# Kernel optimization log

Hardware: AMD Instinct MI355X
Metric: run time of the kernel (lower is better)

## Reference

```python
import jax, jax.numpy as jnp
import numpy as np

BATCH = 2048
INPUT_DIM = 256    # == output_units, since Dense output is fed back into the cell
DEC_UNITS = 1024
OUTPUT_STEPS = 96
OUTPUT_UNITS = 256


def setup_inputs() -> dict:
    key = jax.random.key(0)
    ks = jax.random.split(key, 8)
    scale = 0.05
    return {
        "last_input": jax.random.normal(ks[0], (BATCH, INPUT_DIM), dtype=jnp.float32),
        "h0": jax.random.normal(ks[1], (BATCH, DEC_UNITS), dtype=jnp.float32),
        "c0": jax.random.normal(ks[2], (BATCH, DEC_UNITS), dtype=jnp.float32),
        # LSTMCell params (Keras layout: kernel [in, 4*units], recurrent_kernel [units, 4*units], bias [4*units]; gate order i,f,c,o)
        "Wk": jax.random.normal(ks[3], (INPUT_DIM, 4 * DEC_UNITS), dtype=jnp.float32) * scale,
        "Wr": jax.random.normal(ks[4], (DEC_UNITS, 4 * DEC_UNITS), dtype=jnp.float32) * scale,
        "b": jax.random.normal(ks[5], (4 * DEC_UNITS,), dtype=jnp.float32) * scale,
        # Dense output projection
        "Wd": jax.random.normal(ks[6], (DEC_UNITS, OUTPUT_UNITS), dtype=jnp.float32) * scale,
        "bd": jax.random.normal(ks[7], (OUTPUT_UNITS,), dtype=jnp.float32) * scale,
    }


def reference(last_input, h0, c0, Wk, Wr, b, Wd, bd):
    def step(carry, _):
        x, h, c = carry
        # fused gate GEMM: [B, in] @ [in, 4U] + [B, U] @ [U, 4U]
        z = x @ Wk + h @ Wr + b
        zi, zf, zg, zo = jnp.split(z, 4, axis=-1)  # Keras gate order: i, f, c(g), o
        i = jax.nn.sigmoid(zi)
        f = jax.nn.sigmoid(zf)
        o = jax.nn.sigmoid(zo)
        c_new = f * c + i * jnp.tanh(zg)
        h_new = o * jnp.tanh(c_new)
        pred = h_new @ Wd + bd  # fed back as next step's input
        return (pred, h_new, c_new), pred

    _, preds = jax.lax.scan(step, (last_input, h0, c0), None, length=OUTPUT_STEPS)
    # preds: [T, B, out] -> [B, T, out] (matches tf.transpose(predictions, [1,0,2]))
    return jnp.transpose(preds, (1, 0, 2))
```

## Files before the change

### kernel.cpp

```cpp
#include <hip/hip_runtime.h>
#include <hip/hip_bf16.h>
#include <stdint.h>

#define B_SZ 2048
#define U_SZ 1024
#define G_SZ 4096
#define I_SZ 256
#define O_SZ 256
#define T_SZ 96
#define K1_SZ 1280

typedef _Float16 half8 __attribute__((ext_vector_type(8)));
typedef float float4v __attribute__((ext_vector_type(4)));

__device__ inline float sigm_f(float x) { return 1.0f / (1.0f + __expf(-x)); }
__device__ inline float tanh_f(float x) { return 1.0f - 2.0f / (1.0f + __expf(2.0f * x)); }

__device__ inline short f2h(float x) {
    return __builtin_bit_cast(short, (_Float16)x);
}

__device__ inline void cp16(const void* g, void* l) {
    __builtin_amdgcn_global_load_lds(
        (const __attribute__((address_space(1))) void*)g,
        (__attribute__((address_space(3))) void*)l,
        16, 0, 0);
}


__global__ void transpose_reord(const float* __restrict__ in, float* __restrict__ out, int K) {
    __shared__ float s[32][33];
    int c0 = blockIdx.x * 32, k0 = blockIdx.y * 32;
    int tx = threadIdx.x, ty = threadIdx.y;
#pragma unroll
    for (int i = 0; i < 4; i++)
        s[ty + 8 * i][tx] = in[(long)(k0 + ty + 8 * i) * G_SZ + c0 + tx];
    __syncthreads();
#pragma unroll
    for (int i = 0; i < 4; i++) {
        int cc = ty + 8 * i;
        int c = c0 + cc;
        int n = 4 * (c & 1023) + (c >> 10);
        out[(long)n * K + k0 + tx] = s[tx][cc];
    }
}

__global__ void transpose_f32(const float* __restrict__ in, float* __restrict__ out, int R, int C) {
    __shared__ float s[32][33];
    int c0 = blockIdx.x * 32, r0 = blockIdx.y * 32;
    int tx = threadIdx.x, ty = threadIdx.y;
#pragma unroll
    for (int i = 0; i < 4; i++)
        s[ty + 8 * i][tx] = in[(long)(r0 + ty + 8 * i) * C + c0 + tx];
    __syncthreads();
#pragma unroll
    for (int i = 0; i < 4; i++)
        out[(long)(c0 + ty + 8 * i) * R + r0 + tx] = s[tx][ty + 8 * i];
}

__global__ void transpose_f16(const float* __restrict__ in, short* __restrict__ out, int R, int C) {
    __shared__ float s[32][33];
    int c0 = blockIdx.x * 32, r0 = blockIdx.y * 32;
    int tx = threadIdx.x, ty = threadIdx.y;
#pragma unroll
    for (int i = 0; i < 4; i++)
        s[ty + 8 * i][tx] = in[(long)(r0 + ty + 8 * i) * C + c0 + tx];
    __syncthreads();
#pragma unroll
    for (int i = 0; i < 4; i++)
        out[(long)(c0 + ty + 8 * i) * R + r0 + tx] = f2h(s[tx][ty + 8 * i]);
}

__global__ void cast_f16(const float* __restrict__ in, short* __restrict__ out) {
    long i = (long)blockIdx.x * 256 + threadIdx.x;
    out[i] = f2h(in[i]);
}

__global__ void build_b0t(const float* __restrict__ WkT, const float* __restrict__ WrT,
                          short* __restrict__ B0T) {
    long idx = (long)blockIdx.x * 256 + threadIdx.x;
    long n = idx / K1_SZ, k = idx % K1_SZ;
    float v = (k < I_SZ) ? WkT[n * I_SZ + k] : WrT[n * U_SZ + (k - I_SZ)];
    B0T[idx] = f2h(v);
}

__global__ void build_x0(const float* __restrict__ x0, const float* __restrict__ h0,
                         short* __restrict__ X0) {
    long idx = (long)blockIdx.x * 256 + threadIdx.x;
    long m = idx / K1_SZ, k = idx % K1_SZ;
    float v = (k < I_SZ) ? x0[m * I_SZ + k] : h0[m * U_SZ + (k - I_SZ)];
    X0[idx] = f2h(v);
}

__global__ void build_ber(const float* __restrict__ Wk, const float* __restrict__ b,
                          const float* __restrict__ bd, float* __restrict__ beR,
                          float* __restrict__ bR) {
    int c = blockIdx.x * 256 + threadIdx.x;
    float s = 0.0f;
    for (int p = 0; p < I_SZ; p++) s += bd[p] * Wk[(long)p * G_SZ + c];
    int slot = 4 * (c & 1023) + (c >> 10);
    bR[slot] = b[c];
    beR[slot] = b[c] + s;
}

__device__ __forceinline__ void gemm_core(char* smem, const char* gA, const char* gB,
                                          long Kb, int KI, int w, int l,
                                          float4v (&acc)[4][4]) {
    const int lr = l & 15, lk = l >> 4;
    const int wg = w >> 1, wb = w & 1;
    char* const lA = smem + (w * 32) * 128;
    char* const lB = smem + 32768 + (w * 16) * 128;

    auto stage = [&](int kt, int b) {
        const long go = (long)kt * 128;
        char* dA = lA + b * 49152;
        char* dB = lB + b * 49152;
#pragma unroll
        for (int ci = 0; ci < 4; ++ci) cp16(gA + (long)ci * 8 * Kb + go, dA + ci * 1024);
#pragma unroll
        for (int ci = 0; ci < 2; ++ci) cp16(gB + (long)ci * 8 * Kb + go, dB + ci * 1024);
    };
    auto compute = [&](int b) {
        const char* As = smem + b * 49152;
        const char* Bs = As + 32768;
#pragma unroll
        for (int ks = 0; ks < 2; ++ks) {
            half8 af[4], bf[4];
            const int chunk = (ks * 4 + lk) ^ (lr & 7);
#pragma unroll
            for (int mi = 0; mi < 4; ++mi)
                af[mi] = *(const half8*)(As + (wg * 64 + mi * 16 + lr) * 128 + chunk * 16);
#pragma unroll
            for (int ni = 0; ni < 4; ++ni)
                bf[ni] = *(const half8*)(Bs + (wb * 64 + ni * 16 + lr) * 128 + chunk * 16);
            __builtin_amdgcn_s_setprio(1);
#pragma unroll
            for (int mi = 0; mi < 4; ++mi)
#pragma unroll
                for (int ni = 0; ni < 4; ++ni)
                    acc[mi][ni] = __builtin_amdgcn_mfma_f32_16x16x32_f16(
                        af[mi], bf[ni], acc[mi][ni], 0, 0, 0);
            __builtin_amdgcn_s_setprio(0);
        }
    };

    stage(0, 0);
    stage(1, 1);
    int bc = 0, bs = 2;
    for (int kt = 0; kt < KI; ++kt) {
        if (kt < KI - 1)
            asm volatile("s_waitcnt vmcnt(6) lgkmcnt(0)" ::: "memory");
        else
            asm volatile("s_waitcnt vmcnt(0) lgkmcnt(0)" ::: "memory");
        __builtin_amdgcn_s_barrier();
        asm volatile("" ::: "memory");
        if (kt + 2 < KI) stage(kt + 2, bs);
        compute(bc);
        bc = (bc == 2) ? 0 : bc + 1;
        bs = (bs == 2) ? 0 : bs + 1;
    }
}

__global__ __launch_bounds__(512, 2) void lstm_step(
    const short* __restrict__ A, const short* __restrict__ Bm, int K,
    float* __restrict__ cT, const float* __restrict__ beR, short* __restrict__ hOut) {
    __shared__ char smem[147456];

    const int tid = threadIdx.x;
    const int w = tid >> 6, l = tid & 63;
    const int wg = w >> 1, wb = w & 1;
    const int n_blk = blockIdx.x, m_blk = blockIdx.y;
    const long Kb = (long)K * 2;

    float4v acc[4][4];
#pragma unroll
    for (int i = 0; i < 4; i++)
#pragma unroll
        for (int j = 0; j < 4; j++) acc[i][j] = (float4v)0.0f;

    const int r8 = l >> 3;
    const int s8 = l & 7;
    const int gch = s8 ^ r8;
    const char* gA = (const char*)A + ((long)(n_blk * 256 + w * 32 + r8)) * Kb + gch * 16;
    const char* gB = (const char*)Bm + ((long)(m_blk * 128 + w * 16 + r8)) * Kb + gch * 16;

    gemm_core(smem, gA, gB, Kb, K >> 6, w, l, acc);

    const int lr = l & 15, lk = l >> 4;
    short* hs = (short*)smem;
    __syncthreads();
    const int j_base = n_blk * 64 + wg * 16;
    const int m_base = m_blk * 128 + wb * 64;
#pragma unroll
    for (int mi = 0; mi < 4; ++mi) {
        int j = j_base + mi * 4 + lk;
        float4v bias = *(const float4v*)(beR + 4 * j);
#pragma unroll
        for (int ni = 0; ni < 4; ++ni) {
            int m = m_base + ni * 16 + lr;
            float zi = acc[mi][ni][0] + bias[0];
            float zf = acc[mi][ni][1] + bias[1];
            float zg = acc[mi][ni][2] + bias[2];
            float zo = acc[mi][ni][3] + bias[3];
            float ig = sigm_f(zi), fg = sigm_f(zf), gg = tanh_f(zg), og = sigm_f(zo);
            long cidx = (long)j * B_SZ + m;
            float cn = fg * cT[cidx] + ig * gg;
            cT[cidx] = cn;
            float h = og * tanh_f(cn);
            int mm = wb * 64 + ni * 16 + lr;
            int jj = wg * 16 + mi * 4 + lk;
            hs[mm * 64 + (jj ^ ((mm & 7) << 3))] = f2h(h);
        }
    }
    __syncthreads();
    {
        const int q = tid & 7;
        int rr = tid >> 3;
#pragma unroll
        for (int it = 0; it < 2; ++it, rr += 64) {
            uint4 v = *(const uint4*)(hs + rr * 64 + ((q ^ (rr & 7)) * 8));
            *(uint4*)(hOut + (long)(m_blk * 128 + rr) * U_SZ + n_blk * 64 + q * 8) = v;
        }
    }
}

__global__ __launch_bounds__(512, 2) void dense_out(
    const short* __restrict__ Hm, const short* __restrict__ WdT,
    const float* __restrict__ bd, float* __restrict__ out, int t_fix) {
    __shared__ char smem[147456];

    const int tid = threadIdx.x;
    const int w = tid >> 6, l = tid & 63;
    const int wg = w >> 1, wb = w & 1;
    const int o_blk = blockIdx.x, m_blk = blockIdx.y;
    const long Kb = U_SZ * 2;

    float4v acc[4][4];
#pragma unroll
    for (int i = 0; i < 4; i++)
#pragma unroll
        for (int j = 0; j < 4; j++) acc[i][j] = (float4v)0.0f;

    const int r8 = l >> 3, s8 = l & 7, gch = s8 ^ r8;
    const char* gA = (const char*)Hm + ((long)(m_blk * 256 + w * 32 + r8)) * Kb + gch * 16;
    const char* gB = (const char*)WdT + ((long)(o_blk * 128 + w * 16 + r8)) * Kb + gch * 16;

    gemm_core(smem, gA, gB, Kb, U_SZ >> 6, w, l, acc);

    const int lr = l & 15, lk = l >> 4;
#pragma unroll
    for (int ni = 0; ni < 4; ++ni) {
        int o = o_blk * 128 + wb * 64 + ni * 16 + lr;
        float bo = bd[o];
#pragma unroll
        for (int mi = 0; mi < 4; ++mi) {
#pragma unroll
            for (int r = 0; r < 4; ++r) {
                int m = m_blk * 256 + wg * 64 + mi * 16 + lk * 4 + r;
                int t = (t_fix >= 0) ? t_fix : (m >> 11);
                int b = (t_fix >= 0) ? m : (m & 2047);
                out[(long)b * (T_SZ * O_SZ) + (long)t * O_SZ + o] = acc[mi][ni][r] + bo;
            }
        }
    }
}

__global__ __launch_bounds__(512, 2) void fold_mfma(
    const short* __restrict__ WkTh, const short* __restrict__ Wdh,
    const float* __restrict__ WrT, short* __restrict__ WeT) {
    __shared__ char smem[147456];

    const int tid = threadIdx.x;
    const int w = tid >> 6, l = tid & 63;
    const int wg = w >> 1, wb = w & 1;
    const int n_blk = blockIdx.x, k_blk = blockIdx.y;
    const long Kb = I_SZ * 2;

    float4v acc[4][4];
#pragma unroll
    for (int i = 0; i < 4; i++)
#pragma unroll
        for (int j = 0; j < 4; j++) acc[i][j] = (float4v)0.0f;

    const int r8 = l >> 3, s8 = l & 7, gch = s8 ^ r8;
    const char* gA = (const char*)WkTh + ((long)(n_blk * 256 + w * 32 + r8)) * Kb + gch * 16;
    const char* gB = (const char*)Wdh + ((long)(k_blk * 128 + w * 16 + r8)) * Kb + gch * 16;

    gemm_core(smem, gA, gB, Kb, I_SZ >> 6, w, l, acc);

    const int lr = l & 15, lk = l >> 4;
#pragma unroll
    for (int mi = 0; mi < 4; ++mi)
#pragma unroll
        for (int ni = 0; ni < 4; ++ni)
#pragma unroll
            for (int r = 0; r < 4; ++r) {
                long n = n_blk * 256 + wg * 64 + mi * 16 + lk * 4 + r;
                long k = k_blk * 128 + wb * 64 + ni * 16 + lr;
                WeT[n * U_SZ + k] = f2h(WrT[n * U_SZ + k] + acc[mi][ni][r]);
            }
}

extern "C" void kernel_launch(void* const* d_in, const int* in_sizes, int n_in,
                              void* d_out, int out_size, void* d_ws, size_t ws_size,
                              hipStream_t stream) {
    (void)in_sizes; (void)n_in; (void)out_size;
    const float* x0 = (const float*)d_in[0];
    const float* h0 = (const float*)d_in[1];
    const float* c0 = (const float*)d_in[2];
    const float* Wk = (const float*)d_in[3];
    const float* Wr = (const float*)d_in[4];
    const float* bb = (const float*)d_in[5];
    const float* Wd = (const float*)d_in[6];
    const float* bd = (const float*)d_in[7];
    float* out = (float*)d_out;

    char* p = (char*)d_ws;
    auto alloc = [&](size_t bytes) {
        char* r = p;
        p += (bytes + 255) & ~(size_t)255;
        return r;
    };
    short* WeT = (short*)alloc((size_t)G_SZ * U_SZ * 2);
    short* B0T = (short*)alloc((size_t)G_SZ * K1_SZ * 2);
    short* X0 = (short*)alloc((size_t)B_SZ * K1_SZ * 2);
    short* WdT = (short*)alloc((size_t)O_SZ * U_SZ * 2);
    short* WkTh = (short*)alloc((size_t)G_SZ * I_SZ * 2);
    short* Wdh = (short*)alloc((size_t)U_SZ * I_SZ * 2);
    float* beR = (float*)alloc((size_t)U_SZ * 4 * 4);
    float* bR = (float*)alloc((size_t)U_SZ * 4 * 4);
    float* cT = (float*)alloc((size_t)U_SZ * B_SZ * 4);
    char* R = p;
    const size_t SLAB = (size_t)B_SZ * U_SZ * 2;
    size_t rem = (ws_size > (size_t)(R - (char*)d_ws)) ? ws_size - (size_t)(R - (char*)d_ws) : 0;
    bool hist = rem >= (size_t)T_SZ * SLAB;

    float* WkT = (float*)R;
    float* WrT = (float*)(R + (size_t)G_SZ * I_SZ * 4);

    transpose_reord<<<dim3(G_SZ / 32, I_SZ / 32), dim3(32, 8), 0, stream>>>(Wk, WkT, I_SZ);
    transpose_reord<<<dim3(G_SZ / 32, U_SZ / 32), dim3(32, 8), 0, stream>>>(Wr, WrT, U_SZ);
    cast_f16<<<(G_SZ * I_SZ) / 256, 256, 0, stream>>>(WkT, WkTh);
    cast_f16<<<(U_SZ * I_SZ) / 256, 256, 0, stream>>>(Wd, Wdh);
    fold_mfma<<<dim3(G_SZ / 256, U_SZ / 128), 512, 0, stream>>>(WkTh, Wdh, WrT, WeT);
    build_b0t<<<(int)(((size_t)G_SZ * K1_SZ) / 256), 256, 0, stream>>>(WkT, WrT, B0T);
    build_ber<<<G_SZ / 256, 256, 0, stream>>>(Wk, bb, bd, beR, bR);
    transpose_f16<<<dim3(O_SZ / 32, U_SZ / 32), dim3(32, 8), 0, stream>>>(Wd, WdT, U_SZ, O_SZ);
    transpose_f32<<<dim3(U_SZ / 32, B_SZ / 32), dim3(32, 8), 0, stream>>>(c0, cT, B_SZ, U_SZ);
    build_x0<<<(int)(((size_t)B_SZ * K1_SZ) / 256), 256, 0, stream>>>(x0, h0, X0);

    auto slab = [&](int t) -> short* {
        if (hist) return (short*)(R + (size_t)(t - 1) * SLAB);
        return (short*)(R + (size_t)((t - 1) & 1) * SLAB);
    };

    for (int t = 1; t <= T_SZ; ++t) {
        if (t == 1)
            lstm_step<<<dim3(G_SZ / 256, B_SZ / 128), 512, 0, stream>>>(
                B0T, X0, K1_SZ, cT, bR, slab(1));
        else
            lstm_step<<<dim3(G_SZ / 256, B_SZ / 128), 512, 0, stream>>>(
                WeT, slab(t - 1), U_SZ, cT, beR, slab(t));
        if (!hist)
            dense_out<<<dim3(2, B_SZ / 256), 512, 0, stream>>>(slab(t), WdT, bd, out, t - 1);
    }
    if (hist)
        dense_out<<<dim3(2, (T_SZ * B_SZ) / 256), 512, 0, stream>>>((short*)R, WdT, bd, out, -1);
}
```

Before: 2.737 ms.

## Split GEMM k-tile into two phases and remap blocks for XCD locality

The GEMM main loop is restructured into two half-phases per k-tile. Each phase issues its LDS fragment reads, then half of the next global-to-LDS prefetch, then waits and runs the MFMAs, so loads interleave with compute more finely. Separately, the 2D grid becomes a 1D grid of 256 blocks whose indices map to (n,m) tiles so that blocks on the same XCD share A/B tiles in L2. The trade-off is extra barriers per k-tile and a more delicate vmcnt accounting.

Result: slower. 2.881 ms (+5.2%).

```diff
diff --git a/kernel.cpp b/kernel.cpp
--- a/kernel.cpp
+++ b/kernel.cpp
@@ -111,51 +111,58 @@
     char* const lA = smem + (w * 32) * 128;
     char* const lB = smem + 32768 + (w * 16) * 128;
 
-    auto stage = [&](int kt, int b) {
+    auto stage_half = [&](int kt, int b, int h) {
         const long go = (long)kt * 128;
         char* dA = lA + b * 49152;
         char* dB = lB + b * 49152;
-#pragma unroll
-        for (int ci = 0; ci < 4; ++ci) cp16(gA + (long)ci * 8 * Kb + go, dA + ci * 1024);
-#pragma unroll
-        for (int ci = 0; ci < 2; ++ci) cp16(gB + (long)ci * 8 * Kb + go, dB + ci * 1024);
-    };
-    auto compute = [&](int b) {
-        const char* As = smem + b * 49152;
+        cp16(gA + (long)(2 * h) * 8 * Kb + go, dA + (2 * h) * 1024);
+        cp16(gA + (long)(2 * h + 1) * 8 * Kb + go, dA + (2 * h + 1) * 1024);
+        cp16(gB + (long)h * 8 * Kb + go, dB + h * 1024);
+    };
+    auto stage_full = [&](int kt, int b) {
+        stage_half(kt, b, 0);
+        stage_half(kt, b, 1);
+    };
+
+    auto phase = [&](int bc, int ks, int kt_stage, int bs, int h, int vm) {
+        const char* As = smem + bc * 49152;
         const char* Bs = As + 32768;
-#pragma unroll
-        for (int ks = 0; ks < 2; ++ks) {
-            half8 af[4], bf[4];
-            const int chunk = (ks * 4 + lk) ^ (lr & 7);
-#pragma unroll
-            for (int mi = 0; mi < 4; ++mi)
-                af[mi] = *(const half8*)(As + (wg * 64 + mi * 16 + lr) * 128 + chunk * 16);
+        half8 af[4], bf[4];
+        const int chunk = (ks * 4 + lk) ^ (lr & 7);
+#pragma unroll
+        for (int mi = 0; mi < 4; ++mi)
+            af[mi] = *(const half8*)(As + (wg * 64 + mi * 16 + lr) * 128 + chunk * 16);
+#pragma unroll
+        for (int ni = 0; ni < 4; ++ni)
+            bf[ni] = *(const half8*)(Bs + (wb * 64 + ni * 16 + lr) * 128 + chunk * 16);
+        if (kt_stage < KI) stage_half(kt_stage, bs, h);
+        if (vm == 6) asm volatile("s_waitcnt vmcnt(6)" ::: "memory");
+        else if (vm == 0) asm volatile("s_waitcnt vmcnt(0)" ::: "memory");
+        asm volatile("" ::: "memory");
+        __builtin_amdgcn_s_barrier();
+        asm volatile("s_waitcnt lgkmcnt(0)" ::: "memory");
+        __builtin_amdgcn_s_setprio(1);
+#pragma unroll
+        for (int mi = 0; mi < 4; ++mi)
 #pragma unroll
             for (int ni = 0; ni < 4; ++ni)
-                bf[ni] = *(const half8*)(Bs + (wb * 64 + ni * 16 + lr) * 128 + chunk * 16);
-            __builtin_amdgcn_s_setprio(1);
-#pragma unroll
-            for (int mi = 0; mi < 4; ++mi)
-#pragma unroll
-                for (int ni = 0; ni < 4; ++ni)
-                    acc[mi][ni] = __builtin_amdgcn_mfma_f32_16x16x32_f16(
-                        af[mi], bf[ni], acc[mi][ni], 0, 0, 0);
-            __builtin_amdgcn_s_setprio(0);
-        }
-    };
-
-    stage(0, 0);
-    stage(1, 1);
+                acc[mi][ni] = __builtin_amdgcn_mfma_f32_16x16x32_f16(
+                    af[mi], bf[ni], acc[mi][ni], 0, 0, 0);
+        __builtin_amdgcn_s_setprio(0);
+        asm volatile("" ::: "memory");
+        __builtin_amdgcn_s_barrier();
+    };
+
+    stage_full(0, 0);
+    stage_full(1, 1);
+    asm volatile("s_waitcnt vmcnt(6)" ::: "memory");
+    __builtin_amdgcn_s_barrier();
+
     int bc = 0, bs = 2;
     for (int kt = 0; kt < KI; ++kt) {
-        if (kt < KI - 1)
-            asm volatile("s_waitcnt vmcnt(6) lgkmcnt(0)" ::: "memory");
-        else
-            asm volatile("s_waitcnt vmcnt(0) lgkmcnt(0)" ::: "memory");
-        __builtin_amdgcn_s_barrier();
-        asm volatile("" ::: "memory");
-        if (kt + 2 < KI) stage(kt + 2, bs);
-        compute(bc);
+        int vmB = (kt + 1 < KI) ? ((kt + 2 < KI) ? 6 : 0) : -1;
+        phase(bc, 0, kt + 2, bs, 0, -1);
+        phase(bc, 1, kt + 2, bs, 1, vmB);
         bc = (bc == 2) ? 0 : bc + 1;
         bs = (bs == 2) ? 0 : bs + 1;
     }
@@ -169,7 +176,10 @@
     const int tid = threadIdx.x;
     const int w = tid >> 6, l = tid & 63;
     const int wg = w >> 1, wb = w & 1;
-    const int n_blk = blockIdx.x, m_blk = blockIdx.y;
+    const int bid = blockIdx.x;
+    const int xcd = bid & 7, idx = bid >> 3;
+    const int n_blk = (xcd & 3) * 4 + (idx & 3);
+    const int m_blk = (xcd >> 2) * 8 + (idx >> 2);
     const long Kb = (long)K * 2;
 
     float4v acc[4][4];
@@ -356,10 +366,10 @@
 
     for (int t = 1; t <= T_SZ; ++t) {
         if (t == 1)
-            lstm_step<<<dim3(G_SZ / 256, B_SZ / 128), 512, 0, stream>>>(
+            lstm_step<<<256, 512, 0, stream>>>(
                 B0T, X0, K1_SZ, cT, bR, slab(1));
         else
-            lstm_step<<<dim3(G_SZ / 256, B_SZ / 128), 512, 0, stream>>>(
+            lstm_step<<<256, 512, 0, stream>>>(
                 WeT, slab(t - 1), U_SZ, cT, beR, slab(t));
         if (!hist)
             dense_out<<<dim3(2, B_SZ / 256), 512, 0, stream>>>(slab(t), WdT, bd, out, t - 1);
```

## Fuse LSTM timesteps into persistent kernel with per-row-block atomic barriers

Applied to the files above, without the earlier changes.

Replaces the 96 per-step lstm_step launches with a single persistent kernel of 256 blocks that keeps the cell state and biases in registers. Between steps it synchronises only the 16 blocks sharing a batch row-block through a global atomic counter. It also remaps block indices so each XCD covers a group of tiles, and rewrites dense_out to load MFMA operands directly from global memory instead of staging through LDS. The aim is to remove launch overhead and the repeated c-state loads and stores. The cost is that correctness now depends on all 256 blocks being co-resident (two per CU), or the spin-waits deadlock.

Result: slower. 3.262 ms (+19.2%).

```diff
diff --git a/kernel.cpp b/kernel.cpp
--- a/kernel.cpp
+++ b/kernel.cpp
@@ -102,6 +102,8 @@
     bR[slot] = b[c];
     beR[slot] = b[c] + s;
 }
+
+__global__ void zero_ctr(unsigned int* __restrict__ c) { c[threadIdx.x] = 0u; }
 
 __device__ __forceinline__ void gemm_core(char* smem, const char* gA, const char* gB,
                                           long Kb, int KI, int w, int l,
@@ -161,6 +163,107 @@
     }
 }
 
+__global__ __launch_bounds__(512, 2) void lstm_persist(
+    const short* __restrict__ B0T, const short* __restrict__ X0,
+    const short* __restrict__ WeT, const float* __restrict__ cT,
+    const float* __restrict__ bR, const float* __restrict__ beR,
+    short* __restrict__ slabs, unsigned int* __restrict__ ctr) {
+    __shared__ char smem[147456];
+
+    const int tid = threadIdx.x;
+    const int w = tid >> 6, l = tid & 63;
+    const int wg = w >> 1, wb = w & 1;
+    const int lr = l & 15, lk = l >> 4;
+    const int bid = blockIdx.x;
+    const int xcd = bid & 7, idx = bid >> 3;
+    const int n_blk = (xcd & 3) * 4 + (idx & 3);
+    const int m_blk = (xcd >> 2) * 8 + (idx >> 2);
+
+    const int r8 = l >> 3, s8 = l & 7, gch = s8 ^ r8;
+
+    const int j_base = n_blk * 64 + wg * 16;
+    const int m_base = m_blk * 128 + wb * 64;
+
+    float4v bias4[4];
+    float c4[4][4];
+#pragma unroll
+    for (int mi = 0; mi < 4; ++mi) {
+        int j = j_base + mi * 4 + lk;
+        bias4[mi] = *(const float4v*)(bR + 4 * j);
+#pragma unroll
+        for (int ni = 0; ni < 4; ++ni)
+            c4[mi][ni] = cT[(long)j * B_SZ + m_base + ni * 16 + lr];
+    }
+
+    const size_t SLAB_E = (size_t)B_SZ * U_SZ;
+
+    for (int t = 1; t <= T_SZ; ++t) {
+        const short* Aop = (t == 1) ? B0T : WeT;
+        const short* Bop = (t == 1) ? X0 : (slabs + (size_t)(t - 2) * SLAB_E);
+        const int K = (t == 1) ? K1_SZ : U_SZ;
+        const long Kb = (long)K * 2;
+        const char* gA = (const char*)Aop + ((long)(n_blk * 256 + w * 32 + r8)) * Kb + gch * 16;
+        const char* gB = (const char*)Bop + ((long)(m_blk * 128 + w * 16 + r8)) * Kb + gch * 16;
+
+        float4v acc[4][4];
+#pragma unroll
+        for (int i = 0; i < 4; i++)
+#pragma unroll
+            for (int j = 0; j < 4; j++) acc[i][j] = (float4v)0.0f;
+
+        gemm_core(smem, gA, gB, Kb, K >> 6, w, l, acc);
+
+        short* hs = (short*)smem;
+        __syncthreads();
+#pragma unroll
+        for (int mi = 0; mi < 4; ++mi) {
+#pragma unroll
+            for (int ni = 0; ni < 4; ++ni) {
+                float zi = acc[mi][ni][0] + bias4[mi][0];
+                float zf = acc[mi][ni][1] + bias4[mi][1];
+                float zg = acc[mi][ni][2] + bias4[mi][2];
+                float zo = acc[mi][ni][3] + bias4[mi][3];
+                float ig = sigm_f(zi), fg = sigm_f(zf), gg = tanh_f(zg), og = sigm_f(zo);
+                float cn = fg * c4[mi][ni] + ig * gg;
+                c4[mi][ni] = cn;
+                float h = og * tanh_f(cn);
+                int mm = wb * 64 + ni * 16 + lr;
+                int jj = wg * 16 + mi * 4 + lk;
+                hs[mm * 64 + (jj ^ ((mm & 7) << 3))] = f2h(h);
+            }
+        }
+        __syncthreads();
+        short* hOut = slabs + (size_t)(t - 1) * SLAB_E;
+        {
+            const int q = tid & 7;
+            int rr = tid >> 3;
+#pragma unroll
+            for (int it = 0; it < 2; ++it, rr += 64) {
+                uint4 v = *(const uint4*)(hs + rr * 64 + ((q ^ (rr & 7)) * 8));
+                *(uint4*)(hOut + (long)(m_blk * 128 + rr) * U_SZ + n_blk * 64 + q * 8) = v;
+            }
+        }
+        if (t == 1) {
+#pragma unroll
+            for (int mi = 0; mi < 4; ++mi)
+                bias4[mi] = *(const float4v*)(beR + 4 * (j_base + mi * 4 + lk));
+        }
+        if (t < T_SZ) {
+            __syncthreads();
+            if (tid == 0) {
+                __builtin_amdgcn_fence(__ATOMIC_RELEASE, "agent");
+                __hip_atomic_fetch_add(&ctr[m_blk * 32], 1u, __ATOMIC_RELAXED,
+                                       __HIP_MEMORY_SCOPE_AGENT);
+                const unsigned int tgt = 16u * (unsigned int)t;
+                while (__hip_atomic_load(&ctr[m_blk * 32], __ATOMIC_RELAXED,
+                                         __HIP_MEMORY_SCOPE_AGENT) < tgt)
+                    __builtin_amdgcn_s_sleep(4);
+            }
+            __syncthreads();
+        }
+    }
+}
+
 __global__ __launch_bounds__(512, 2) void lstm_step(
     const short* __restrict__ A, const short* __restrict__ Bm, int K,
     float* __restrict__ cT, const float* __restrict__ beR, short* __restrict__ hOut) {
@@ -169,7 +272,10 @@
     const int tid = threadIdx.x;
     const int w = tid >> 6, l = tid & 63;
     const int wg = w >> 1, wb = w & 1;
-    const int n_blk = blockIdx.x, m_blk = blockIdx.y;
+    const int bid = blockIdx.x;
+    const int xcd = bid & 7, idx = bid >> 3;
+    const int n_blk = (xcd & 3) * 4 + (idx & 3);
+    const int m_blk = (xcd >> 2) * 8 + (idx >> 2);
     const long Kb = (long)K * 2;
 
     float4v acc[4][4];
@@ -178,9 +284,7 @@
 #pragma unroll
         for (int j = 0; j < 4; j++) acc[i][j] = (float4v)0.0f;
 
-    const int r8 = l >> 3;
-    const int s8 = l & 7;
-    const int gch = s8 ^ r8;
+    const int r8 = l >> 3, s8 = l & 7, gch = s8 ^ r8;
     const char* gA = (const char*)A + ((long)(n_blk * 256 + w * 32 + r8)) * Kb + gch * 16;
     const char* gB = (const char*)Bm + ((long)(m_blk * 128 + w * 16 + r8)) * Kb + gch * 16;
 
@@ -227,11 +331,10 @@
 __global__ __launch_bounds__(512, 2) void dense_out(
     const short* __restrict__ Hm, const short* __restrict__ WdT,
     const float* __restrict__ bd, float* __restrict__ out, int t_fix) {
-    __shared__ char smem[147456];
-
     const int tid = threadIdx.x;
     const int w = tid >> 6, l = tid & 63;
     const int wg = w >> 1, wb = w & 1;
+    const int lr = l & 15, lk = l >> 4;
     const int o_blk = blockIdx.x, m_blk = blockIdx.y;
     const long Kb = U_SZ * 2;
 
@@ -241,13 +344,50 @@
 #pragma unroll
         for (int j = 0; j < 4; j++) acc[i][j] = (float4v)0.0f;
 
-    const int r8 = l >> 3, s8 = l & 7, gch = s8 ^ r8;
-    const char* gA = (const char*)Hm + ((long)(m_blk * 256 + w * 32 + r8)) * Kb + gch * 16;
-    const char* gB = (const char*)WdT + ((long)(o_blk * 128 + w * 16 + r8)) * Kb + gch * 16;
-
-    gemm_core(smem, gA, gB, Kb, U_SZ >> 6, w, l, acc);
-
-    const int lr = l & 15, lk = l >> 4;
+    const char* pa[4];
+    const char* pb[4];
+#pragma unroll
+    for (int i = 0; i < 4; ++i) {
+        pa[i] = (const char*)Hm + ((long)(m_blk * 256 + wg * 64 + i * 16 + lr)) * Kb + lk * 16;
+        pb[i] = (const char*)WdT + ((long)(o_blk * 128 + wb * 64 + i * 16 + lr)) * Kb + lk * 16;
+    }
+
+    half8 a0[4], b0[4], a1[4], b1[4];
+#pragma unroll
+    for (int i = 0; i < 4; ++i) {
+        a0[i] = *(const half8*)(pa[i]);
+        b0[i] = *(const half8*)(pb[i]);
+    }
+#pragma unroll
+    for (int s = 0; s < 32; s += 2) {
+        if (s + 1 < 32) {
+#pragma unroll
+            for (int i = 0; i < 4; ++i) {
+                a1[i] = *(const half8*)(pa[i] + (s + 1) * 64);
+                b1[i] = *(const half8*)(pb[i] + (s + 1) * 64);
+            }
+        }
+#pragma unroll
+        for (int mi = 0; mi < 4; ++mi)
+#pragma unroll
+            for (int ni = 0; ni < 4; ++ni)
+                acc[mi][ni] = __builtin_amdgcn_mfma_f32_16x16x32_f16(
+                    a0[mi], b0[ni], acc[mi][ni], 0, 0, 0);
+        if (s + 2 < 32) {
+#pragma unroll
+            for (int i = 0; i < 4; ++i) {
+                a0[i] = *(const half8*)(pa[i] + (s + 2) * 64);
+                b0[i] = *(const half8*)(pb[i] + (s + 2) * 64);
+            }
+        }
+#pragma unroll
+        for (int mi = 0; mi < 4; ++mi)
+#pragma unroll
+            for (int ni = 0; ni < 4; ++ni)
+                acc[mi][ni] = __builtin_amdgcn_mfma_f32_16x16x32_f16(
+                    a1[mi], b1[ni], acc[mi][ni], 0, 0, 0);
+    }
+
 #pragma unroll
     for (int ni = 0; ni < 4; ++ni) {
         int o = o_blk * 128 + wb * 64 + ni * 16 + lr;
@@ -330,6 +470,7 @@
     float* beR = (float*)alloc((size_t)U_SZ * 4 * 4);
     float* bR = (float*)alloc((size_t)U_SZ * 4 * 4);
     float* cT = (float*)alloc((size_t)U_SZ * B_SZ * 4);
+    unsigned int* ctr = (unsigned int*)alloc(2048);
     char* R = p;
     const size_t SLAB = (size_t)B_SZ * U_SZ * 2;
     size_t rem = (ws_size > (size_t)(R - (char*)d_ws)) ? ws_size - (size_t)(R - (char*)d_ws) : 0;
@@ -338,6 +479,7 @@
     float* WkT = (float*)R;
     float* WrT = (float*)(R + (size_t)G_SZ * I_SZ * 4);
 
+    zero_ctr<<<1, 512, 0, stream>>>(ctr);
     transpose_reord<<<dim3(G_SZ / 32, I_SZ / 32), dim3(32, 8), 0, stream>>>(Wk, WkT, I_SZ);
     transpose_reord<<<dim3(G_SZ / 32, U_SZ / 32), dim3(32, 8), 0, stream>>>(Wr, WrT, U_SZ);
     cast_f16<<<(G_SZ * I_SZ) / 256, 256, 0, stream>>>(WkT, WkTh);
@@ -349,21 +491,19 @@
     transpose_f32<<<dim3(U_SZ / 32, B_SZ / 32), dim3(32, 8), 0, stream>>>(c0, cT, B_SZ, U_SZ);
     build_x0<<<(int)(((size_t)B_SZ * K1_SZ) / 256), 256, 0, stream>>>(x0, h0, X0);
 
-    auto slab = [&](int t) -> short* {
-        if (hist) return (short*)(R + (size_t)(t - 1) * SLAB);
-        return (short*)(R + (size_t)((t - 1) & 1) * SLAB);
-    };
-
-    for (int t = 1; t <= T_SZ; ++t) {
-        if (t == 1)
-            lstm_step<<<dim3(G_SZ / 256, B_SZ / 128), 512, 0, stream>>>(
-                B0T, X0, K1_SZ, cT, bR, slab(1));
-        else
-            lstm_step<<<dim3(G_SZ / 256, B_SZ / 128), 512, 0, stream>>>(
-                WeT, slab(t - 1), U_SZ, cT, beR, slab(t));
-        if (!hist)
+    if (hist) {
+        lstm_persist<<<256, 512, 0, stream>>>(B0T, X0, WeT, cT, bR, beR, (short*)R, ctr);
+        dense_out<<<dim3(2, (T_SZ * B_SZ) / 256), 512, 0, stream>>>((short*)R, WdT, bd, out, -1);
+    } else {
+        auto slab = [&](int t) -> short* {
+            return (short*)(R + (size_t)((t - 1) & 1) * SLAB);
+        };
+        for (int t = 1; t <= T_SZ; ++t) {
+            if (t == 1)
+                lstm_step<<<256, 512, 0, stream>>>(B0T, X0, K1_SZ, cT, bR, slab(1));
+            else
+                lstm_step<<<256, 512, 0, stream>>>(WeT, slab(t - 1), U_SZ, cT, beR, slab(t));
             dense_out<<<dim3(2, B_SZ / 256), 512, 0, stream>>>(slab(t), WdT, bd, out, t - 1);
-    }
-    if (hist)
-        dense_out<<<dim3(2, (T_SZ * B_SZ) / 256), 512, 0, stream>>>((short*)R, WdT, bd, out, -1);
-}
+        }
+    }
+}
```

## Pace GEMM k-loop across blocks per XCD with atomic counters and remap blocks

Applied to the files above, without the earlier changes.

Replaces the 2D grid with a 1D grid and remaps block ids so that each XCD owns a contiguous 4x8 tile region of the gate GEMM, which is meant to improve L2 reuse of shared A/B tiles. Every four k-iterations, each block increments a per-XCD atomic counter and spin-waits until all 32 blocks on that XCD reach the same point. This keeps co-resident blocks in lockstep so their tile loads hit in L2. The spin barrier assumes all 32 blocks per XCD are co-resident and that blocks map to XCDs round-robin; if either fails it can stall or deadlock, and the waits add sync overhead.

New measurement: 3.021 ms. +10.4%, slower.

```diff
diff --git a/kernel.cpp b/kernel.cpp
--- a/kernel.cpp
+++ b/kernel.cpp
@@ -102,6 +102,8 @@
     bR[slot] = b[c];
     beR[slot] = b[c] + s;
 }
+
+__global__ void zero_ctr(unsigned int* __restrict__ c) { c[threadIdx.x] = 0u; }
 
 __device__ __forceinline__ void gemm_core(char* smem, const char* gA, const char* gB,
                                           long Kb, int KI, int w, int l,
@@ -161,15 +163,91 @@
     }
 }
 
+__device__ __forceinline__ void gemm_core_paced(char* smem, const char* gA, const char* gB,
+                                                long Kb, int KI, int w, int l,
+                                                float4v (&acc)[4][4], int tid, int xcd,
+                                                unsigned int* pace, int sync_base) {
+    const int lr = l & 15, lk = l >> 4;
+    const int wg = w >> 1, wb = w & 1;
+    char* const lA = smem + (w * 32) * 128;
+    char* const lB = smem + 32768 + (w * 16) * 128;
+
+    auto stage = [&](int kt, int b) {
+        const long go = (long)kt * 128;
+        char* dA = lA + b * 49152;
+        char* dB = lB + b * 49152;
+#pragma unroll
+        for (int ci = 0; ci < 4; ++ci) cp16(gA + (long)ci * 8 * Kb + go, dA + ci * 1024);
+#pragma unroll
+        for (int ci = 0; ci < 2; ++ci) cp16(gB + (long)ci * 8 * Kb + go, dB + ci * 1024);
+    };
+    auto compute = [&](int b) {
+        const char* As = smem + b * 49152;
+        const char* Bs = As + 32768;
+#pragma unroll
+        for (int ks = 0; ks < 2; ++ks) {
+            half8 af[4], bf[4];
+            const int chunk = (ks * 4 + lk) ^ (lr & 7);
+#pragma unroll
+            for (int mi = 0; mi < 4; ++mi)
+                af[mi] = *(const half8*)(As + (wg * 64 + mi * 16 + lr) * 128 + chunk * 16);
+#pragma unroll
+            for (int ni = 0; ni < 4; ++ni)
+                bf[ni] = *(const half8*)(Bs + (wb * 64 + ni * 16 + lr) * 128 + chunk * 16);
+            __builtin_amdgcn_s_setprio(1);
+#pragma unroll
+            for (int mi = 0; mi < 4; ++mi)
+#pragma unroll
+                for (int ni = 0; ni < 4; ++ni)
+                    acc[mi][ni] = __builtin_amdgcn_mfma_f32_16x16x32_f16(
+                        af[mi], bf[ni], acc[mi][ni], 0, 0, 0);
+            __builtin_amdgcn_s_setprio(0);
+        }
+    };
+
+    stage(0, 0);
+    stage(1, 1);
+    int bc = 0, bs = 2;
+    for (int kt = 0; kt < KI; ++kt) {
+        if ((kt & 3) == 0 && kt != 0) {
+            asm volatile("" ::: "memory");
+            if (tid == 0) {
+                const unsigned int tgt = 32u * (unsigned int)(sync_base + (kt >> 2));
+                __hip_atomic_fetch_add(&pace[xcd * 32], 1u, __ATOMIC_RELAXED,
+                                       __HIP_MEMORY_SCOPE_AGENT);
+                while (__hip_atomic_load(&pace[xcd * 32], __ATOMIC_RELAXED,
+                                         __HIP_MEMORY_SCOPE_AGENT) < tgt)
+                    __builtin_amdgcn_s_sleep(1);
+            }
+            __builtin_amdgcn_s_barrier();
+            asm volatile("" ::: "memory");
+        }
+        if (kt < KI - 1)
+            asm volatile("s_waitcnt vmcnt(6) lgkmcnt(0)" ::: "memory");
+        else
+            asm volatile("s_waitcnt vmcnt(0) lgkmcnt(0)" ::: "memory");
+        __builtin_amdgcn_s_barrier();
+        asm volatile("" ::: "memory");
+        if (kt + 2 < KI) stage(kt + 2, bs);
+        compute(bc);
+        bc = (bc == 2) ? 0 : bc + 1;
+        bs = (bs == 2) ? 0 : bs + 1;
+    }
+}
+
 __global__ __launch_bounds__(512, 2) void lstm_step(
     const short* __restrict__ A, const short* __restrict__ Bm, int K,
-    float* __restrict__ cT, const float* __restrict__ beR, short* __restrict__ hOut) {
+    float* __restrict__ cT, const float* __restrict__ beR, short* __restrict__ hOut,
+    unsigned int* __restrict__ pace, int sync_base) {
     __shared__ char smem[147456];
 
     const int tid = threadIdx.x;
     const int w = tid >> 6, l = tid & 63;
     const int wg = w >> 1, wb = w & 1;
-    const int n_blk = blockIdx.x, m_blk = blockIdx.y;
+    const int bid = blockIdx.x;
+    const int xcd = bid & 7, idx = bid >> 3;
+    const int n_blk = (xcd & 3) * 4 + (idx & 3);
+    const int m_blk = (xcd >> 2) * 8 + (idx >> 2);
     const long Kb = (long)K * 2;
 
     float4v acc[4][4];
@@ -178,13 +256,11 @@
 #pragma unroll
         for (int j = 0; j < 4; j++) acc[i][j] = (float4v)0.0f;
 
-    const int r8 = l >> 3;
-    const int s8 = l & 7;
-    const int gch = s8 ^ r8;
+    const int r8 = l >> 3, s8 = l & 7, gch = s8 ^ r8;
     const char* gA = (const char*)A + ((long)(n_blk * 256 + w * 32 + r8)) * Kb + gch * 16;
     const char* gB = (const char*)Bm + ((long)(m_blk * 128 + w * 16 + r8)) * Kb + gch * 16;
 
-    gemm_core(smem, gA, gB, Kb, K >> 6, w, l, acc);
+    gemm_core_paced(smem, gA, gB, Kb, K >> 6, w, l, acc, tid, xcd, pace, sync_base);
 
     const int lr = l & 15, lk = l >> 4;
     short* hs = (short*)smem;
@@ -330,6 +406,7 @@
     float* beR = (float*)alloc((size_t)U_SZ * 4 * 4);
     float* bR = (float*)alloc((size_t)U_SZ * 4 * 4);
     float* cT = (float*)alloc((size_t)U_SZ * B_SZ * 4);
+    unsigned int* pace = (unsigned int*)alloc(1024);
     char* R = p;
     const size_t SLAB = (size_t)B_SZ * U_SZ * 2;
     size_t rem = (ws_size > (size_t)(R - (char*)d_ws)) ? ws_size - (size_t)(R - (char*)d_ws) : 0;
@@ -338,6 +415,7 @@
     float* WkT = (float*)R;
     float* WrT = (float*)(R + (size_t)G_SZ * I_SZ * 4);
 
+    zero_ctr<<<1, 256, 0, stream>>>(pace);
     transpose_reord<<<dim3(G_SZ / 32, I_SZ / 32), dim3(32, 8), 0, stream>>>(Wk, WkT, I_SZ);
     transpose_reord<<<dim3(G_SZ / 32, U_SZ / 32), dim3(32, 8), 0, stream>>>(Wr, WrT, U_SZ);
     cast_f16<<<(G_SZ * I_SZ) / 256, 256, 0, stream>>>(WkT, WkTh);
@@ -354,13 +432,17 @@
         return (short*)(R + (size_t)((t - 1) & 1) * SLAB);
     };
 
+    int sb = 0;
     for (int t = 1; t <= T_SZ; ++t) {
-        if (t == 1)
-            lstm_step<<<dim3(G_SZ / 256, B_SZ / 128), 512, 0, stream>>>(
-                B0T, X0, K1_SZ, cT, bR, slab(1));
-        else
-            lstm_step<<<dim3(G_SZ / 256, B_SZ / 128), 512, 0, stream>>>(
-                WeT, slab(t - 1), U_SZ, cT, beR, slab(t));
+        if (t == 1) {
+            lstm_step<<<256, 512, 0, stream>>>(
+                B0T, X0, K1_SZ, cT, bR, slab(1), pace, sb);
+            sb += ((K1_SZ >> 6) - 1) >> 2;
+        } else {
+            lstm_step<<<256, 512, 0, stream>>>(
+                WeT, slab(t - 1), U_SZ, cT, beR, slab(t), pace, sb);
+            sb += ((U_SZ >> 6) - 1) >> 2;
+        }
         if (!hist)
             dense_out<<<dim3(2, B_SZ / 256), 512, 0, stream>>>(slab(t), WdT, bd, out, t - 1);
     }
```
